# Kernel tuning notes

Measured on AMD Instinct MI355X. Metric: run time of the kernel, lower is better.

## Reference

```python
import jax, jax.numpy as jnp
import numpy as np

D_MODEL = 1024
NHEAD = 16
HEAD_DIM = D_MODEL // NHEAD
B, S = 4, 2048
LN_EPS = 1e-5


def setup_inputs() -> dict:
    key = jax.random.key(0)
    ks = jax.random.split(key, 16)
    def lin(k, fin, fout):
        # torch nn.Linear default init scale ~ 1/sqrt(fin)
        s = 1.0 / np.sqrt(fin)
        kw, kb = jax.random.split(k)
        W = jax.random.uniform(kw, (fin, fout), jnp.float32, -s, s)
        b = jax.random.uniform(kb, (fout,), jnp.float32, -s, s)
        return W, b
    Wq, bq = lin(ks[0], D_MODEL, D_MODEL)
    Wk, bk = lin(ks[1], D_MODEL, D_MODEL)
    Wv, bv = lin(ks[2], D_MODEL, D_MODEL)
    Wo, bo = lin(ks[3], D_MODEL, D_MODEL)
    W1, b1 = lin(ks[4], D_MODEL, 2 * D_MODEL)
    W2, b2 = lin(ks[5], 2 * D_MODEL, D_MODEL)
    return {
        "query": jax.random.normal(ks[6], (B, S, D_MODEL), jnp.float32),
        "key": jax.random.normal(ks[7], (B, S, D_MODEL), jnp.float32),
        "value": jax.random.normal(ks[8], (B, S, D_MODEL), jnp.float32),
        "mask": jnp.ones((1, 1, S, S), dtype=bool),
        "Wq": Wq, "bq": bq, "Wk": Wk, "bk": bk, "Wv": Wv, "bv": bv,
        "Wo": Wo, "bo": bo,
        "ln_g": jnp.ones((D_MODEL,), jnp.float32),
        "ln_b": jnp.zeros((D_MODEL,), jnp.float32),
        "W1": W1, "b1": b1, "W2": W2, "b2": b2,
    }


def _layer_norm(x, g, b):
    mu = jnp.mean(x, axis=-1, keepdims=True)
    var = jnp.mean(jnp.square(x - mu), axis=-1, keepdims=True)
    return (x - mu) * jax.lax.rsqrt(var + LN_EPS) * g + b


def reference(query, key, value, mask, Wq, bq, Wk, bk, Wv, bv, Wo, bo,
              ln_g, ln_b, W1, b1, W2, b2):
    Bq, Sq, _ = query.shape
    # projections -> [B, H, S, hd]
    def split_heads(x):
        return x.reshape(Bq, -1, NHEAD, HEAD_DIM).transpose(0, 2, 1, 3)
    q = split_heads(query @ Wq + bq)
    k = split_heads(key @ Wk + bk)
    v = split_heads(value @ Wv + bv)
    scores = jnp.einsum("bhqd,bhkd->bhqk", q, k) / jnp.sqrt(
        jnp.asarray(HEAD_DIM, q.dtype))
    scores = jnp.where(mask, scores, jnp.asarray(-jnp.inf, scores.dtype))
    probs = jax.nn.softmax(scores, axis=-1)  # dropout is identity at eval
    ctx = jnp.einsum("bhqk,bhkd->bhqd", probs, v)
    ctx = ctx.transpose(0, 2, 1, 3).reshape(Bq, Sq, D_MODEL)
    out = ctx @ Wo + bo
    # residual with (pre-projection) query input, then layer norm
    out = _layer_norm(query + out, ln_g, ln_b)
    # FFN: Linear -> ReLU -> Linear
    out = jax.nn.relu(out @ W1 + b1) @ W2 + b2
    return out
```

## Files before the change

kernel.cpp:

```cpp
#include <hip/hip_runtime.h>

typedef unsigned short u16;
typedef u16 u16x4 __attribute__((ext_vector_type(4)));
typedef u16 u16x8 __attribute__((ext_vector_type(8)));
typedef __bf16 bf16x8 __attribute__((ext_vector_type(8)));
typedef float f32x4 __attribute__((ext_vector_type(4)));

__device__ __forceinline__ u16 f2bf(float f) {
  return __builtin_bit_cast(u16, (__bf16)f);
}

__device__ __forceinline__ bf16x8 ldbf8(const u16* p) {
  union { u16x8 u; bf16x8 b; } t;
  t.u = *(const u16x8*)p;
  return t.b;
}

__device__ __forceinline__ bf16x8 cat44(u16x4 a, u16x4 b) {
  union { u16x4 h[2]; bf16x8 v; } t;
  t.h[0] = a; t.h[1] = b;
  return t.v;
}

#if __has_builtin(__builtin_amdgcn_exp2f)
#define EXP2(x) __builtin_amdgcn_exp2f(x)
#else
#define EXP2(x) exp2f(x)
#endif

#define MFMA16(a, b, c) __builtin_amdgcn_mfma_f32_16x16x32_bf16(a, b, c, 0, 0, 0)

__device__ __forceinline__ void gl16(const u16* g, u16* l) {
  __builtin_amdgcn_global_load_lds(
      (const __attribute__((address_space(1))) void*)g,
      (__attribute__((address_space(3))) void*)l, 16, 0, 0);
}

struct PrepDesc { const float* W; u16* WT; int K; int N; };
struct Prep { PrepDesc d[6]; const float* cs[3]; u16* cd[3]; };

__global__ __launch_bounds__(256, 4) void prep_k(Prep p) {
  const int z = blockIdx.z;
  if (z < 6) {
    PrepDesc dd = p.d[z];
    const int n0 = blockIdx.x * 32, k0 = blockIdx.y * 32;
    if (n0 >= dd.N || k0 >= dd.K) return;
    __shared__ float tt[32][33];
    const int tx = threadIdx.x & 31, ty = threadIdx.x >> 5;
#pragma unroll
    for (int i = 0; i < 4; i++) {
      int k = ty + i * 8;
      tt[k][tx] = dd.W[(size_t)(k0 + k) * dd.N + n0 + tx];
    }
    __syncthreads();
#pragma unroll
    for (int i = 0; i < 4; i++) {
      int n = ty + i * 8;
      dd.WT[(size_t)(n0 + n) * dd.K + k0 + tx] = f2bf(tt[tx][n]);
    }
  } else {
    const float* src = p.cs[z - 6];
    u16* dst = p.cd[z - 6];
    size_t base = ((size_t)(blockIdx.y * 64 + blockIdx.x)) * 2048 + threadIdx.x * 4;
#pragma unroll
    for (int j = 0; j < 2; j++) {
      f32x4 v = *(const f32x4*)(src + base + j * 1024);
      u16x4 o;
      o.x = f2bf(v.x); o.y = f2bf(v.y); o.z = f2bf(v.z); o.w = f2bf(v.w);
      *(u16x4*)(dst + base + j * 1024) = o;
    }
  }
}

struct Acc44 { f32x4 a[4][4]; };

__device__ __forceinline__ void stage_unit(const u16* src, u16* dst, int K,
                                           int w, int rsub, int c8x) {
#pragma unroll
  for (int j = 0; j < 2; j++) {
    const int chunk = w * 2 + j;
    const int row = chunk * 8 + rsub;
    gl16(src + (size_t)row * K + c8x, dst + chunk * 512);
  }
}

__device__ __forceinline__ void gemm_core256(const u16* __restrict__ A,
                                             const u16* __restrict__ B,
                                             int m0, int n0, int K,
                                             int tid, u16* ldsA, u16* ldsB,
                                             Acc44& acc) {
#pragma unroll
  for (int mi = 0; mi < 4; mi++)
#pragma unroll
    for (int ni = 0; ni < 4; ni++) acc.a[mi][ni] = 0.f;

  const int lane = tid & 63, w = tid >> 6;
  const int c = lane & 15, quad = lane >> 4;
  const int rsub = lane >> 3;
  const int c8x = ((lane & 7) ^ rsub) * 8;
  const int s0 = (quad ^ (c & 7)) * 8;
  const int s1 = ((4 + quad) ^ (c & 7)) * 8;
  const int wm = (w >> 1) * 64, wn = (w & 1) * 64;

  const u16* Ab = A + (size_t)m0 * K;
  const u16* Bb = B + (size_t)n0 * K;

  const int NT = K >> 6;
  stage_unit(Ab, ldsA, K, w, rsub, c8x);
  stage_unit(Ab + (size_t)128 * K, ldsA + 8192, K, w, rsub, c8x);
  stage_unit(Bb, ldsB, K, w, rsub, c8x);

  for (int t = 0; t < NT; t++) {
    const int cur = t & 1, nxt = cur ^ 1;
    const u16* A_c = ldsA + cur * 16384;
    const u16* B_c = ldsB + cur * 8192;
    u16* A_n = ldsA + nxt * 16384;
    u16* B_n = ldsB + nxt * 8192;
    const u16* Ag = Ab + (t + 1) * 64;
    const u16* Bg = Bb + (t + 1) * 64;
    const bool hn = (t + 1 < NT);

    bf16x8 bg[4], af[2];

    if (hn) {
      stage_unit(Ag, A_n, K, w, rsub, c8x);
      asm volatile("s_waitcnt vmcnt(2)" ::: "memory");
    } else {
      asm volatile("s_waitcnt vmcnt(0)" ::: "memory");
    }
    __builtin_amdgcn_s_barrier();
#pragma unroll
    for (int ni = 0; ni < 4; ni++)
      bg[ni] = ldbf8(&B_c[(wn + ni * 16 + c) * 64 + s0]);
    af[0] = ldbf8(&A_c[(wm + 0 * 16 + c) * 64 + s0]);
    af[1] = ldbf8(&A_c[(wm + 1 * 16 + c) * 64 + s0]);
    __builtin_amdgcn_s_setprio(1);
#pragma unroll
    for (int mi = 0; mi < 2; mi++)
#pragma unroll
      for (int ni = 0; ni < 4; ni++)
        acc.a[mi][ni] = MFMA16(af[mi], bg[ni], acc.a[mi][ni]);
    __builtin_amdgcn_s_setprio(0);
    __builtin_amdgcn_s_barrier();

    af[0] = ldbf8(&A_c[(wm + 2 * 16 + c) * 64 + s0]);
    af[1] = ldbf8(&A_c[(wm + 3 * 16 + c) * 64 + s0]);
    if (hn) stage_unit(Ag + (size_t)128 * K, A_n + 8192, K, w, rsub, c8x);
    __builtin_amdgcn_s_barrier();
    __builtin_amdgcn_s_setprio(1);
#pragma unroll
    for (int mi = 0; mi < 2; mi++)
#pragma unroll
      for (int ni = 0; ni < 4; ni++)
        acc.a[2 + mi][ni] = MFMA16(af[mi], bg[ni], acc.a[2 + mi][ni]);
    __builtin_amdgcn_s_setprio(0);
    __builtin_amdgcn_s_barrier();

#pragma unroll
    for (int ni = 0; ni < 4; ni++)
      bg[ni] = ldbf8(&B_c[(wn + ni * 16 + c) * 64 + s1]);
    af[0] = ldbf8(&A_c[(wm + 0 * 16 + c) * 64 + s1]);
    af[1] = ldbf8(&A_c[(wm + 1 * 16 + c) * 64 + s1]);
    if (hn) stage_unit(Bg, B_n, K, w, rsub, c8x);
    __builtin_amdgcn_s_barrier();
    __builtin_amdgcn_s_setprio(1);
#pragma unroll
    for (int mi = 0; mi < 2; mi++)
#pragma unroll
      for (int ni = 0; ni < 4; ni++)
        acc.a[mi][ni] = MFMA16(af[mi], bg[ni], acc.a[mi][ni]);
    __builtin_amdgcn_s_setprio(0);
    __builtin_amdgcn_s_barrier();

    af[0] = ldbf8(&A_c[(wm + 2 * 16 + c) * 64 + s1]);
    af[1] = ldbf8(&A_c[(wm + 3 * 16 + c) * 64 + s1]);
    __builtin_amdgcn_s_barrier();
    __builtin_amdgcn_s_setprio(1);
#pragma unroll
    for (int mi = 0; mi < 2; mi++)
#pragma unroll
      for (int ni = 0; ni < 4; ni++)
        acc.a[2 + mi][ni] = MFMA16(af[mi], bg[ni], acc.a[2 + mi][ni]);
    __builtin_amdgcn_s_setprio(0);
    __builtin_amdgcn_s_barrier();
  }
}

__global__ __launch_bounds__(512, 2) void qkv_k(const u16* __restrict__ qb,
                                                const u16* __restrict__ kb,
                                                const u16* __restrict__ vb,
                                                const u16* __restrict__ WqT,
                                                const u16* __restrict__ WkT,
                                                const u16* __restrict__ WvT,
                                                const float* __restrict__ bq,
                                                const float* __restrict__ bk,
                                                const float* __restrict__ bv,
                                                u16* __restrict__ qp,
                                                u16* __restrict__ kp,
                                                u16* __restrict__ vp) {
  const int tid = threadIdx.x;
  const int lane = tid & 63, w = tid >> 6;
  const int c = lane & 15, quad = lane >> 4;
  const int z = blockIdx.y;
  int f = blockIdx.x;
  f = (f & 7) * 32 + (f >> 3);
  int bx, by;
  if (z < 2) { bx = f & 7;  by = f >> 3; }
  else       { bx = f & 63; by = f >> 6; }
  const int n0 = bx * 128, m0 = by * 256;
  const u16 *A, *B;
  if (z < 2) { A = z ? kb : qb; B = z ? WkT : WqT; }
  else       { A = WvT; B = vb; }
  const int wm = (w >> 1) * 64, wn = (w & 1) * 64;

  __shared__ __attribute__((aligned(16))) u16 ldsA[2 * 16384];
  __shared__ __attribute__((aligned(16))) u16 ldsB[2 * 8192];
  Acc44 acc;
  gemm_core256(A, B, m0, n0, 1024, tid, ldsA, ldsB, acc);

#pragma unroll
  for (int mi = 0; mi < 4; mi++)
#pragma unroll
    for (int ni = 0; ni < 4; ni++)
#pragma unroll
      for (int r = 0; r < 4; r++) {
        int row = m0 + wm + mi * 16 + quad * 4 + r;
        int col = n0 + wn + ni * 16 + c;
        if (z < 2) {
          const float* bias = z ? bk : bq;
          u16* out = z ? kp : qp;
          float v = acc.a[mi][ni][r] + bias[col];
          int b = row >> 11, s = row & 2047, h = col >> 6, d = col & 63;
          out[(((size_t)(b * 16 + h) * 2048 + s) << 6) + d] = f2bf(v);
        } else {
          float v = acc.a[mi][ni][r] + bv[row];
          int b = col >> 11, s = col & 2047, h = row >> 6, d = row & 63;
          vp[(((size_t)(b * 16 + h) * 64 + d) << 11) + s] = f2bf(v);
        }
      }
}

template <int MODE>
__global__ __launch_bounds__(512, 2) void gemm_k(const u16* __restrict__ A,
                                                 const u16* __restrict__ B,
                                                 const float* __restrict__ bias,
                                                 const float* __restrict__ resid,
                                                 void* __restrict__ Out,
                                                 int M, int N, int K) {
  const int tid = threadIdx.x;
  const int lane = tid & 63, w = tid >> 6;
  const int c = lane & 15, quad = lane >> 4;
  const int nx = gridDim.x;
  const int nwg = nx * gridDim.y;
  int f = blockIdx.x + nx * blockIdx.y;
  f = (f & 7) * (nwg >> 3) + (f >> 3);
  const int bx = f % nx, by = f / nx;
  const int n0 = bx * 128, m0 = by * 256;
  const int wm = (w >> 1) * 64, wn = (w & 1) * 64;

  __shared__ __attribute__((aligned(16))) u16 ldsA[2 * 16384];
  __shared__ __attribute__((aligned(16))) u16 ldsB[2 * 8192];
  Acc44 acc;
  gemm_core256(A, B, m0, n0, K, tid, ldsA, ldsB, acc);

#pragma unroll
  for (int mi = 0; mi < 4; mi++)
#pragma unroll
    for (int ni = 0; ni < 4; ni++)
#pragma unroll
      for (int r = 0; r < 4; r++) {
        int row = m0 + wm + mi * 16 + quad * 4 + r;
        int col = n0 + wn + ni * 16 + c;
        float v = acc.a[mi][ni][r] + bias[col];
        if constexpr (MODE == 1) {
          v += resid[(size_t)row * N + col];
          ((float*)Out)[(size_t)row * N + col] = v;
        } else if constexpr (MODE == 2) {
          v = fmaxf(v, 0.f);
          ((u16*)Out)[(size_t)row * N + col] = f2bf(v);
        } else {
          ((float*)Out)[(size_t)row * N + col] = v;
        }
      }
}

__global__ __launch_bounds__(256, 4) void attn_k(const u16* __restrict__ Qp,
                                                 const u16* __restrict__ Kp,
                                                 const u16* __restrict__ Vt,
                                                 u16* __restrict__ ctx) {
  const int tid = threadIdx.x, lane = tid & 63, w = tid >> 6;
  const int c = lane & 15, quad = lane >> 4;
  const int bh = blockIdx.x, qt = blockIdx.y;
  const int b = bh >> 4, h = bh & 15;

  __shared__ u16 lds[2 * 64 * 72];
  u16* Kt = lds;
  u16* Vs = lds + 64 * 72;

  const u16* Qb = Qp + ((size_t)bh * 2048 + qt * 128 + w * 32) * 64;
  bf16x8 aq[2][2];
#pragma unroll
  for (int st = 0; st < 2; st++)
#pragma unroll
    for (int ks = 0; ks < 2; ks++)
      aq[st][ks] = ldbf8(Qb + (st * 16 + c) * 64 + ks * 32 + quad * 8);

  const float SC = 0.18033688011112042f;
  f32x4 o[2][4];
  float rs[2] = {0.f, 0.f};
#pragma unroll
  for (int st = 0; st < 2; st++)
#pragma unroll
    for (int dt = 0; dt < 4; dt++) o[st][dt] = 0.f;

  const u16* Kb0 = Kp + (size_t)bh * 2048 * 64;
  const u16* Vb0 = Vt + (size_t)bh * 64 * 2048;
  const int sr = tid >> 3, sc8 = (tid & 7) * 8;

  u16x8 kr[2], vr[2];
#pragma unroll
  for (int j = 0; j < 2; j++) {
    kr[j] = *(const u16x8*)(Kb0 + ((size_t)(j * 32 + sr)) * 64 + sc8);
    vr[j] = *(const u16x8*)(Vb0 + (size_t)(j * 32 + sr) * 2048 + sc8);
  }

  for (int kt = 0; kt < 32; kt++) {
    __syncthreads();
#pragma unroll
    for (int j = 0; j < 2; j++) {
      *(u16x8*)&Kt[(j * 32 + sr) * 72 + sc8] = kr[j];
      *(u16x8*)&Vs[(j * 32 + sr) * 72 + sc8] = vr[j];
    }
    __syncthreads();
    if (kt < 31) {
#pragma unroll
      for (int j = 0; j < 2; j++) {
        kr[j] = *(const u16x8*)(Kb0 + ((size_t)(kt + 1) * 64 + j * 32 + sr) * 64 + sc8);
        vr[j] = *(const u16x8*)(Vb0 + (size_t)(j * 32 + sr) * 2048 + (kt + 1) * 64 + sc8);
      }
    }

    f32x4 sT[2][4];
#pragma unroll
    for (int ct = 0; ct < 4; ct++) {
      bf16x8 ka0 = ldbf8(&Kt[(ct * 16 + c) * 72 + 0 + quad * 8]);
      bf16x8 ka1 = ldbf8(&Kt[(ct * 16 + c) * 72 + 32 + quad * 8]);
#pragma unroll
      for (int st = 0; st < 2; st++) {
        f32x4 t = 0.f;
        t = __builtin_amdgcn_mfma_f32_16x16x32_bf16(ka0, aq[st][0], t, 0, 0, 0);
        t = __builtin_amdgcn_mfma_f32_16x16x32_bf16(ka1, aq[st][1], t, 0, 0, 0);
        sT[st][ct] = t;
      }
    }

    u16x4 pb[2][4];
#pragma unroll
    for (int st = 0; st < 2; st++)
#pragma unroll
      for (int ct = 0; ct < 4; ct++)
#pragma unroll
        for (int r = 0; r < 4; r++) {
          float pf = EXP2(sT[st][ct][r] * SC);
          rs[st] += pf;
          pb[st][ct][r] = f2bf(pf);
        }

#pragma unroll
    for (int kh = 0; kh < 2; kh++) {
      bf16x8 pB[2];
#pragma unroll
      for (int st = 0; st < 2; st++) pB[st] = cat44(pb[st][2 * kh], pb[st][2 * kh + 1]);
#pragma unroll
      for (int dt = 0; dt < 4; dt++) {
        const u16* vrow = &Vs[(dt * 16 + c) * 72 + kh * 32 + quad * 4];
        bf16x8 A8 = cat44(*(const u16x4*)vrow, *(const u16x4*)(vrow + 16));
#pragma unroll
        for (int st = 0; st < 2; st++)
          o[st][dt] = __builtin_amdgcn_mfma_f32_16x16x32_bf16(A8, pB[st], o[st][dt], 0, 0, 0);
      }
    }
  }

  float inv[2];
#pragma unroll
  for (int st = 0; st < 2; st++) {
    float r = rs[st];
    r += __shfl_xor(r, 16);
    r += __shfl_xor(r, 32);
    inv[st] = 1.0f / r;
  }

  __syncthreads();
  u16* Ob = lds + w * 2304;
#pragma unroll
  for (int st = 0; st < 2; st++)
#pragma unroll
    for (int dt = 0; dt < 4; dt++)
#pragma unroll
      for (int r = 0; r < 4; r++)
        Ob[(st * 16 + c) * 72 + dt * 16 + quad * 4 + r] = f2bf(o[st][dt][r] * inv[st]);
#pragma unroll
  for (int j = 0; j < 4; j++) {
    int r_ = j * 8 + (lane >> 3), dc = (lane & 7) * 8;
    u16x8 v = *(const u16x8*)&Ob[r_ * 72 + dc];
    int s_ = qt * 128 + w * 32 + r_;
    *(u16x8*)&ctx[((size_t)b * 2048 + s_) * 1024 + h * 64 + dc] = v;
  }
}

__global__ __launch_bounds__(256, 4) void ln_k(const float* __restrict__ X,
                                               const float* __restrict__ g,
                                               const float* __restrict__ bt,
                                               u16* __restrict__ out) {
  const int row = blockIdx.x, tid = threadIdx.x;
  const float* x = X + (size_t)row * 1024;
  f32x4 v = *(const f32x4*)(x + tid * 4);
  float s = v.x + v.y + v.z + v.w;
  float sq = v.x * v.x + v.y * v.y + v.z * v.z + v.w * v.w;
#pragma unroll
  for (int off = 1; off < 64; off <<= 1) {
    s += __shfl_xor(s, off);
    sq += __shfl_xor(sq, off);
  }
  __shared__ float red[4][2];
  if ((tid & 63) == 0) { red[tid >> 6][0] = s; red[tid >> 6][1] = sq; }
  __syncthreads();
  s = red[0][0] + red[1][0] + red[2][0] + red[3][0];
  sq = red[0][1] + red[1][1] + red[2][1] + red[3][1];
  float mu = s * (1.0f / 1024.0f);
  float var = sq * (1.0f / 1024.0f) - mu * mu;
  float rstd = rsqrtf(var + 1e-5f);
#pragma unroll
  for (int j = 0; j < 4; j++) {
    int col = tid * 4 + j;
    out[(size_t)row * 1024 + col] = f2bf((v[j] - mu) * rstd * g[col] + bt[col]);
  }
}

extern "C" void kernel_launch(void* const* d_in, const int* in_sizes, int n_in,
                              void* d_out, int out_size, void* d_ws, size_t ws_size,
                              hipStream_t stream) {
  const float* query = (const float*)d_in[0];
  const float* key_  = (const float*)d_in[1];
  const float* value = (const float*)d_in[2];
  const float* Wq = (const float*)d_in[4];  const float* bq = (const float*)d_in[5];
  const float* Wk = (const float*)d_in[6];  const float* bk = (const float*)d_in[7];
  const float* Wv = (const float*)d_in[8];  const float* bv = (const float*)d_in[9];
  const float* Wo = (const float*)d_in[10]; const float* bo = (const float*)d_in[11];
  const float* ln_g = (const float*)d_in[12]; const float* ln_b = (const float*)d_in[13];
  const float* W1 = (const float*)d_in[14]; const float* b1 = (const float*)d_in[15];
  const float* W2 = (const float*)d_in[16]; const float* b2 = (const float*)d_in[17];

  const size_t MB = 1u << 20;
  if (ws_size < 112 * MB) return;
  char* ws = (char*)d_ws;
  u16* WqT = (u16*)(ws + 0 * MB);
  u16* WkT = (u16*)(ws + 2 * MB);
  u16* WvT = (u16*)(ws + 4 * MB);
  u16* WoT = (u16*)(ws + 6 * MB);
  u16* W1T = (u16*)(ws + 8 * MB);
  u16* W2T = (u16*)(ws + 12 * MB);
  u16* qb  = (u16*)(ws + 16 * MB);
  u16* kb  = (u16*)(ws + 32 * MB);
  u16* vb  = (u16*)(ws + 48 * MB);
  u16* qp  = (u16*)(ws + 64 * MB);
  u16* kp  = (u16*)(ws + 80 * MB);
  u16* vp  = (u16*)(ws + 96 * MB);
  u16* ctxp = (u16*)(ws + 16 * MB);
  float* resid = (float*)(ws + 32 * MB);
  u16* xb = (u16*)(ws + 64 * MB);
  u16* hb = (u16*)(ws + 80 * MB);

  Prep p;
  p.d[0] = {Wq, WqT, 1024, 1024}; p.d[1] = {Wk, WkT, 1024, 1024};
  p.d[2] = {Wv, WvT, 1024, 1024}; p.d[3] = {Wo, WoT, 1024, 1024};
  p.d[4] = {W1, W1T, 1024, 2048}; p.d[5] = {W2, W2T, 2048, 1024};
  p.cs[0] = query; p.cs[1] = key_; p.cs[2] = value;
  p.cd[0] = qb;    p.cd[1] = kb;   p.cd[2] = vb;
  prep_k<<<dim3(64, 64, 9), 256, 0, stream>>>(p);

  qkv_k<<<dim3(256, 3), 512, 0, stream>>>(qb, kb, vb, WqT, WkT, WvT,
                                          bq, bk, bv, qp, kp, vp);

  attn_k<<<dim3(64, 16), 256, 0, stream>>>(qp, kp, vp, ctxp);

  gemm_k<1><<<dim3(8, 32), 512, 0, stream>>>(ctxp, WoT, bo, query, resid, 8192, 1024, 1024);

  ln_k<<<8192, 256, 0, stream>>>(resid, ln_g, ln_b, xb);

  gemm_k<2><<<dim3(16, 32), 512, 0, stream>>>(xb, W1T, b1, nullptr, hb, 8192, 2048, 1024);
  gemm_k<3><<<dim3(8, 32), 512, 0, stream>>>(hb, W2T, b2, nullptr, (float*)d_out, 8192, 1024, 2048);
}
```

Baseline: 521.6 us.

## Triple-buffer GEMM LDS tiles with two-ahead prefetch and coarser MFMA phases

Restructures the shared GEMM core from double-buffered to triple-buffered LDS, so global loads for tile t+2 are issued while tile t is being computed. Each K-tile now runs two larger MFMA phases (all four M sub-tiles at once) instead of four smaller ones, which removes barriers and raises register-level reuse. The A staging now covers 256 rows in one call. Shared memory grows to 144 KB per block, so launch bounds drop to one block per CU. That gives up the overlap previously available between two co-resident blocks.

```diff
diff --git a/kernel.cpp b/kernel.cpp
--- a/kernel.cpp
+++ b/kernel.cpp
@@ -74,8 +74,17 @@
 
 struct Acc44 { f32x4 a[4][4]; };
 
-__device__ __forceinline__ void stage_unit(const u16* src, u16* dst, int K,
-                                           int w, int rsub, int c8x) {
+__device__ __forceinline__ void stage_unitA(const u16* src, u16* dst, int K,
+                                            int w, int rsub, int c8x) {
+#pragma unroll
+  for (int j = 0; j < 4; j++) {
+    const int chunk = w * 4 + j;
+    const int row = chunk * 8 + rsub;
+    gl16(src + (size_t)row * K + c8x, dst + chunk * 512);
+  }
+}
+__device__ __forceinline__ void stage_unitB(const u16* src, u16* dst, int K,
+                                            int w, int rsub, int c8x) {
 #pragma unroll
   for (int j = 0; j < 2; j++) {
     const int chunk = w * 2 + j;
@@ -106,87 +115,64 @@
   const u16* Bb = B + (size_t)n0 * K;
 
   const int NT = K >> 6;
-  stage_unit(Ab, ldsA, K, w, rsub, c8x);
-  stage_unit(Ab + (size_t)128 * K, ldsA + 8192, K, w, rsub, c8x);
-  stage_unit(Bb, ldsB, K, w, rsub, c8x);
+  stage_unitA(Ab, ldsA, K, w, rsub, c8x);
+  stage_unitB(Bb, ldsB, K, w, rsub, c8x);
+  stage_unitA(Ab + 64, ldsA + 16384, K, w, rsub, c8x);
+  stage_unitB(Bb + 64, ldsB + 8192, K, w, rsub, c8x);
+  asm volatile("s_waitcnt vmcnt(6)" ::: "memory");
+  __builtin_amdgcn_s_barrier();
 
   for (int t = 0; t < NT; t++) {
-    const int cur = t & 1, nxt = cur ^ 1;
-    const u16* A_c = ldsA + cur * 16384;
-    const u16* B_c = ldsB + cur * 8192;
-    u16* A_n = ldsA + nxt * 16384;
-    u16* B_n = ldsB + nxt * 8192;
-    const u16* Ag = Ab + (t + 1) * 64;
-    const u16* Bg = Bb + (t + 1) * 64;
-    const bool hn = (t + 1 < NT);
-
-    bf16x8 bg[4], af[2];
-
-    if (hn) {
-      stage_unit(Ag, A_n, K, w, rsub, c8x);
-      asm volatile("s_waitcnt vmcnt(2)" ::: "memory");
-    } else {
-      asm volatile("s_waitcnt vmcnt(0)" ::: "memory");
-    }
-    __builtin_amdgcn_s_barrier();
+    const u16* A_c = ldsA + (t % 3) * 16384;
+    const u16* B_c = ldsB + (t % 3) * 8192;
+    u16* A_n = ldsA + ((t + 2) % 3) * 16384;
+    u16* B_n = ldsB + ((t + 2) % 3) * 8192;
+    const bool hn = (t + 2 < NT);
+
+    bf16x8 af[4], bg[4];
+
+#pragma unroll
+    for (int mi = 0; mi < 4; mi++)
+      af[mi] = ldbf8(&A_c[(wm + mi * 16 + c) * 64 + s0]);
 #pragma unroll
     for (int ni = 0; ni < 4; ni++)
       bg[ni] = ldbf8(&B_c[(wn + ni * 16 + c) * 64 + s0]);
-    af[0] = ldbf8(&A_c[(wm + 0 * 16 + c) * 64 + s0]);
-    af[1] = ldbf8(&A_c[(wm + 1 * 16 + c) * 64 + s0]);
+    if (hn) stage_unitA(Ab + (t + 2) * 64, A_n, K, w, rsub, c8x);
+    __builtin_amdgcn_s_barrier();
     __builtin_amdgcn_s_setprio(1);
 #pragma unroll
-    for (int mi = 0; mi < 2; mi++)
+    for (int mi = 0; mi < 4; mi++)
 #pragma unroll
       for (int ni = 0; ni < 4; ni++)
         acc.a[mi][ni] = MFMA16(af[mi], bg[ni], acc.a[mi][ni]);
     __builtin_amdgcn_s_setprio(0);
     __builtin_amdgcn_s_barrier();
 
-    af[0] = ldbf8(&A_c[(wm + 2 * 16 + c) * 64 + s0]);
-    af[1] = ldbf8(&A_c[(wm + 3 * 16 + c) * 64 + s0]);
-    if (hn) stage_unit(Ag + (size_t)128 * K, A_n + 8192, K, w, rsub, c8x);
+#pragma unroll
+    for (int mi = 0; mi < 4; mi++)
+      af[mi] = ldbf8(&A_c[(wm + mi * 16 + c) * 64 + s1]);
+#pragma unroll
+    for (int ni = 0; ni < 4; ni++)
+      bg[ni] = ldbf8(&B_c[(wn + ni * 16 + c) * 64 + s1]);
+    if (hn) {
+      stage_unitB(Bb + (t + 2) * 64, B_n, K, w, rsub, c8x);
+      asm volatile("s_waitcnt vmcnt(6)" ::: "memory");
+    } else {
+      asm volatile("s_waitcnt vmcnt(0)" ::: "memory");
+    }
     __builtin_amdgcn_s_barrier();
     __builtin_amdgcn_s_setprio(1);
 #pragma unroll
-    for (int mi = 0; mi < 2; mi++)
-#pragma unroll
-      for (int ni = 0; ni < 4; ni++)
-        acc.a[2 + mi][ni] = MFMA16(af[mi], bg[ni], acc.a[2 + mi][ni]);
-    __builtin_amdgcn_s_setprio(0);
-    __builtin_amdgcn_s_barrier();
-
-#pragma unroll
-    for (int ni = 0; ni < 4; ni++)
-      bg[ni] = ldbf8(&B_c[(wn + ni * 16 + c) * 64 + s1]);
-    af[0] = ldbf8(&A_c[(wm + 0 * 16 + c) * 64 + s1]);
-    af[1] = ldbf8(&A_c[(wm + 1 * 16 + c) * 64 + s1]);
-    if (hn) stage_unit(Bg, B_n, K, w, rsub, c8x);
-    __builtin_amdgcn_s_barrier();
-    __builtin_amdgcn_s_setprio(1);
-#pragma unroll
-    for (int mi = 0; mi < 2; mi++)
+    for (int mi = 0; mi < 4; mi++)
 #pragma unroll
       for (int ni = 0; ni < 4; ni++)
         acc.a[mi][ni] = MFMA16(af[mi], bg[ni], acc.a[mi][ni]);
     __builtin_amdgcn_s_setprio(0);
     __builtin_amdgcn_s_barrier();
-
-    af[0] = ldbf8(&A_c[(wm + 2 * 16 + c) * 64 + s1]);
-    af[1] = ldbf8(&A_c[(wm + 3 * 16 + c) * 64 + s1]);
-    __builtin_amdgcn_s_barrier();
-    __builtin_amdgcn_s_setprio(1);
-#pragma unroll
-    for (int mi = 0; mi < 2; mi++)
-#pragma unroll
-      for (int ni = 0; ni < 4; ni++)
-        acc.a[2 + mi][ni] = MFMA16(af[mi], bg[ni], acc.a[2 + mi][ni]);
-    __builtin_amdgcn_s_setprio(0);
-    __builtin_amdgcn_s_barrier();
-  }
-}
-
-__global__ __launch_bounds__(512, 2) void qkv_k(const u16* __restrict__ qb,
+  }
+}
+
+__global__ __launch_bounds__(512, 1) void qkv_k(const u16* __restrict__ qb,
                                                 const u16* __restrict__ kb,
                                                 const u16* __restrict__ vb,
                                                 const u16* __restrict__ WqT,
@@ -213,8 +199,8 @@
   else       { A = WvT; B = vb; }
   const int wm = (w >> 1) * 64, wn = (w & 1) * 64;
 
-  __shared__ __attribute__((aligned(16))) u16 ldsA[2 * 16384];
-  __shared__ __attribute__((aligned(16))) u16 ldsB[2 * 8192];
+  __shared__ __attribute__((aligned(16))) u16 ldsA[3 * 16384];
+  __shared__ __attribute__((aligned(16))) u16 ldsB[3 * 8192];
   Acc44 acc;
   gemm_core256(A, B, m0, n0, 1024, tid, ldsA, ldsB, acc);
 
@@ -241,7 +227,7 @@
 }
 
 template <int MODE>
-__global__ __launch_bounds__(512, 2) void gemm_k(const u16* __restrict__ A,
+__global__ __launch_bounds__(512, 1) void gemm_k(const u16* __restrict__ A,
                                                  const u16* __restrict__ B,
                                                  const float* __restrict__ bias,
                                                  const float* __restrict__ resid,
@@ -258,8 +244,8 @@
   const int n0 = bx * 128, m0 = by * 256;
   const int wm = (w >> 1) * 64, wn = (w & 1) * 64;
 
-  __shared__ __attribute__((aligned(16))) u16 ldsA[2 * 16384];
-  __shared__ __attribute__((aligned(16))) u16 ldsB[2 * 8192];
+  __shared__ __attribute__((aligned(16))) u16 ldsA[3 * 16384];
+  __shared__ __attribute__((aligned(16))) u16 ldsB[3 * 8192];
   Acc44 acc;
   gemm_core256(A, B, m0, n0, K, tid, ldsA, ldsB, acc);
 
```

After: 465.4 us. -10.8%, faster.
